# Optimization experiments

Measured on AMD Instinct MI355X. Metric: run time of the kernel, lower is better.

The kernel has to match this reference:

```python
import jax, jax.numpy as jnp
import numpy as np
from jax import lax

W_WIN = 7  # window size from init_kwargs


def _dwconv(x, k):
    """Depthwise 2D conv, SAME padding, kernel k: [C,1,kh,kw] (OIHW)."""
    C = x.shape[1]
    p = k.shape[-1] // 2
    return lax.conv_general_dilated(
        x, k, window_strides=(1, 1), padding=[(p, p), (p, p)],
        feature_group_count=C, dimension_numbers=("NCHW", "OIHW", "NCHW"))


def setup_inputs() -> dict:
    key = jax.random.key(0)
    ks = jax.random.split(key, 6)
    B, C, H, Wd = 1, 48, 56, 56
    x = jax.random.normal(ks[0], (B, C, H, Wd), dtype=jnp.float32)
    # small init scale keeps the softmax logits (dot/49) in a sane range
    w3 = jax.random.normal(ks[1], (C, 1, 3, 3), dtype=jnp.float32) * 0.1
    w5 = jax.random.normal(ks[2], (C, 1, 5, 5), dtype=jnp.float32) * 0.1
    w7 = jax.random.normal(ks[3], (C, 1, 7, 7), dtype=jnp.float32) * 0.1
    pw = jax.random.normal(ks[4], (C, 3 * C, 1, 1), dtype=jnp.float32) * 0.05
    pb = jax.random.normal(ks[5], (C,), dtype=jnp.float32) * 0.01
    return {"x": x, "w3": w3, "w5": w5, "w7": w7, "pw": pw, "pb": pb}


def reference(x, w3, w5, w7, pw, pb):
    B, C, H, Wd = x.shape
    w = W_WIN
    # multi-scale depthwise branch, concat on channels -> [B, 3C, H, W]
    y = jnp.concatenate([_dwconv(x, w3), _dwconv(x, w5), _dwconv(x, w7)], axis=1)
    pad_h = (-H) % w
    pad_w = (-Wd) % w
    if pad_h or pad_w:  # static Python ints -> jit-safe
        y = jnp.pad(y, ((0, 0), (0, 0), (0, pad_h), (0, pad_w)), mode="reflect")
    Hp, Wp = y.shape[2], y.shape[3]
    nH, nW = Hp // w, Wp // w
    C3 = 3 * C
    # equivalent to torch unfold(2,w,w).unfold(3,w,w).permute(0,1,2,4,3,5)
    # .reshape(B,3C,nH*nW,w*w): same row-major linearization
    yw = y.reshape(B, C3, nH * nW, w * w)
    # rows: (B, nH*nW, 3C) flattened -> N x (w*w)
    yf = yw.transpose(0, 2, 1, 3).reshape(B * nH * nW * C3, w * w)
    # full N x N self-attention over all rows (faithful to the original)
    attn = jax.nn.softmax((yf @ yf.T) / (w * w), axis=-1)
    y_hat = (attn @ yf).reshape(B, nH, nW, C3, w, w)
    y_hat = y_hat.transpose(0, 3, 1, 4, 2, 5).reshape(B, C3, nH * w, nW * w)
    y_hat = y_hat[:, :, :H, :Wd]
    # 1x1 projection 3C -> C, plus residual
    out = jnp.einsum("oi,bihw->bohw", pw[:, :, 0, 0], y_hat) + pb[None, :, None, None]
    return x + out
```

## Files before the change

kernel.cpp:

```cpp
#include <hip/hip_runtime.h>

typedef unsigned int uint;
typedef unsigned short ushort;
typedef __attribute__((ext_vector_type(8))) short bf16x8;
typedef __attribute__((ext_vector_type(4))) float f32x4;

#define C_IN   48
#define C3     144
#define HW     56
#define SSP    3136
#define DW     49
#define DPAD   64
#define NROWS  9216

#define NSPLIT 12
#define TPS    12

#define CSC 0.02944245f

#define YF_B    0
#define YFT_B   1179648
#define OPART_B 2359296
#define ESUM_B  (OPART_B + NSPLIT * DW * NROWS * 2)

__device__ __forceinline__ ushort f32_to_bf16_rne(float x) {
  uint b = __float_as_uint(x);
  b += 0x7fffu + ((b >> 16) & 1u);
  return (ushort)(b >> 16);
}
__device__ __forceinline__ float bf16_to_f32(ushort u) {
  return __uint_as_float(((uint)u) << 16);
}
__device__ __forceinline__ void async_copy16(const void* g, void* l) {
  __builtin_amdgcn_global_load_lds(
      (const __attribute__((address_space(1))) unsigned int*)g,
      (__attribute__((address_space(3))) unsigned int*)l, 16, 0, 0);
}

__global__ __launch_bounds__(256) void conv_kernel(
    const float* __restrict__ x, const float* __restrict__ w3,
    const float* __restrict__ w5, const float* __restrict__ w7,
    ushort* __restrict__ yf, ushort* __restrict__ yfT) {
  __shared__ ushort tile[4][64];
  const int tid = threadIdx.x;
  const int idx = blockIdx.x * 256 + tid;
  const int r = idx >> 6, t = idx & 63;
  const int rr = r & 3;
  const int r0 = r & ~3;

  ushort ov = 0;
  if (t < DW) {
    int g = r / C3, c3 = r - g * C3;
    int flat = g * DW + t;
    int h = flat / HW, w = flat - h * HW;
    int grp = c3 / C_IN, c = c3 - grp * C_IN;
    const float* wk; int ks;
    if (grp == 0)      { wk = w3 + c * 9;  ks = 3; }
    else if (grp == 1) { wk = w5 + c * 25; ks = 5; }
    else               { wk = w7 + c * 49; ks = 7; }
    int p = ks >> 1;
    const float* xc = x + c * SSP;
    float val = 0.f;
    for (int dy = 0; dy < ks; dy++) {
      int hy = h + dy - p;
      if (hy < 0 || hy >= HW) continue;
      const float* xr = xc + hy * HW;
      const float* wr = wk + dy * ks;
      for (int dx = 0; dx < ks; dx++) {
        int wx = w + dx - p;
        if (wx < 0 || wx >= HW) continue;
        val += xr[wx] * wr[dx];
      }
    }
    ov = f32_to_bf16_rne(val);
  }
  yf[idx] = ov;
  tile[rr][t] = ov;
  __syncthreads();

  if (tid < 64) {
    ushort4 v;
    if (tid == 56) {
      v.x = 0x3F80; v.y = 0x3F80; v.z = 0x3F80; v.w = 0x3F80;
    } else {
      v.x = tile[0][tid]; v.y = tile[1][tid];
      v.z = tile[2][tid]; v.w = tile[3][tid];
    }
    *(ushort4*)&yfT[tid * NROWS + r0] = v;
  }
}

__global__ __launch_bounds__(512, 4) void attn_kernel(
    const ushort* __restrict__ yf, const ushort* __restrict__ yfT,
    ushort* __restrict__ opart, float* __restrict__ esum_g) {
  __shared__ __align__(16) char smem[69632];

  const int tid = threadIdx.x;
  const int w = tid >> 6, lane = tid & 63;
  const int q = lane >> 4, c = lane & 15;
  const int m0 = blockIdx.x * 256 + w * 32;
  const int sp = blockIdx.y;
  ushort* Pm = (ushort*)(smem + 32768) + w * (32 * 72);

  bf16x8 qf[2][2];
#pragma unroll
  for (int mt = 0; mt < 2; mt++)
#pragma unroll
    for (int ds = 0; ds < 2; ds++) {
      bf16x8 raw = *(const bf16x8*)&yf[(m0 + mt * 16 + c) * 64 + ds * 32 + q * 8];
      short tmp[8];
#pragma unroll
      for (int j = 0; j < 8; j++)
        tmp[j] = (short)f32_to_bf16_rne(bf16_to_f32((ushort)raw[j]) * CSC);
      qf[mt][ds] = *(bf16x8*)tmp;
    }

  f32x4 o[4][2];
#pragma unroll
  for (int dt = 0; dt < 4; dt++)
#pragma unroll
    for (int mt = 0; mt < 2; mt++) o[dt][mt] = (f32x4)0.f;

  {
    const int k0 = (sp * TPS) * 64;
    async_copy16(yf + (k0 + lane) * 64 + w * 8, smem + w * 1024);
    async_copy16(yfT + lane * NROWS + k0 + w * 8, smem + 16384 + w * 1024);
  }
  __syncthreads();

  for (int it = 0; it < TPS; it++) {
    const int cur = it & 1;
    if (it + 1 < TPS) {
      const int k1 = (sp * TPS + it + 1) * 64;
      async_copy16(yf + (k1 + lane) * 64 + w * 8,
                   smem + (cur ^ 1) * 8192 + w * 1024);
      async_copy16(yfT + lane * NROWS + k1 + w * 8,
                   smem + 16384 + (cur ^ 1) * 8192 + w * 1024);
    }

    const char* Kb = smem + cur * 8192;
    const char* Vb = smem + 16384 + cur * 8192;

    f32x4 s[4][2];
#pragma unroll
    for (int nt = 0; nt < 4; nt++) {
      bf16x8 a0 = *(const bf16x8*)(Kb + q * 1024 + (nt * 16 + c) * 16);
      bf16x8 a1 = *(const bf16x8*)(Kb + (4 + q) * 1024 + (nt * 16 + c) * 16);
      s[nt][0] = (f32x4)0.f; s[nt][1] = (f32x4)0.f;
      s[nt][0] = __builtin_amdgcn_mfma_f32_16x16x32_bf16(a0, qf[0][0], s[nt][0], 0, 0, 0);
      s[nt][1] = __builtin_amdgcn_mfma_f32_16x16x32_bf16(a0, qf[1][0], s[nt][1], 0, 0, 0);
      s[nt][0] = __builtin_amdgcn_mfma_f32_16x16x32_bf16(a1, qf[0][1], s[nt][0], 0, 0, 0);
      s[nt][1] = __builtin_amdgcn_mfma_f32_16x16x32_bf16(a1, qf[1][1], s[nt][1], 0, 0, 0);
    }

#pragma unroll
    for (int nt = 0; nt < 4; nt++)
#pragma unroll
      for (int mt = 0; mt < 2; mt++) {
        f32x4 sv = s[nt][mt];
        float p0 = __builtin_amdgcn_exp2f(sv[0]);
        float p1 = __builtin_amdgcn_exp2f(sv[1]);
        float p2 = __builtin_amdgcn_exp2f(sv[2]);
        float p3 = __builtin_amdgcn_exp2f(sv[3]);
        uint d0 = (__float_as_uint(p0) >> 16) | (__float_as_uint(p1) & 0xffff0000u);
        uint d1 = (__float_as_uint(p2) >> 16) | (__float_as_uint(p3) & 0xffff0000u);
        *(uint2*)&Pm[(mt * 16 + c) * 72 + nt * 16 + q * 4] = make_uint2(d0, d1);
      }

    bf16x8 bp[2][2];
#pragma unroll
    for (int mt = 0; mt < 2; mt++)
#pragma unroll
      for (int nc = 0; nc < 2; nc++)
        bp[mt][nc] = *(const bf16x8*)&Pm[(mt * 16 + c) * 72 + nc * 32 + q * 8];
#pragma unroll
    for (int dt = 0; dt < 4; dt++) {
      bf16x8 v0 = *(const bf16x8*)(Vb + q * 1024 + (dt * 16 + c) * 16);
      bf16x8 v1 = *(const bf16x8*)(Vb + (4 + q) * 1024 + (dt * 16 + c) * 16);
      o[dt][0] = __builtin_amdgcn_mfma_f32_16x16x32_bf16(v0, bp[0][0], o[dt][0], 0, 0, 0);
      o[dt][1] = __builtin_amdgcn_mfma_f32_16x16x32_bf16(v0, bp[1][0], o[dt][1], 0, 0, 0);
      o[dt][0] = __builtin_amdgcn_mfma_f32_16x16x32_bf16(v1, bp[0][1], o[dt][0], 0, 0, 0);
      o[dt][1] = __builtin_amdgcn_mfma_f32_16x16x32_bf16(v1, bp[1][1], o[dt][1], 0, 0, 0);
    }

    if (it + 1 < TPS) __syncthreads();
  }

#pragma unroll
  for (int dt = 0; dt < 4; dt++)
#pragma unroll
    for (int mt = 0; mt < 2; mt++)
#pragma unroll
      for (int r = 0; r < 4; r++) {
        int d = dt * 16 + q * 4 + r;
        int m = m0 + mt * 16 + c;
        float v = o[dt][mt][r];
        if (d < DW) {
          opart[(sp * DW + d) * NROWS + m] = f32_to_bf16_rne(v);
        } else if (d == 56) {
          esum_g[sp * NROWS + m] = v;
        }
      }
}

__global__ __launch_bounds__(256) void fuse_pw_kernel(
    const ushort* __restrict__ opart, const float* __restrict__ esum_g,
    const float* __restrict__ x, const float* __restrict__ pw,
    const float* __restrict__ pb, float* __restrict__ out) {
  __shared__ float vb[7 * 145];
  __shared__ float inv_es[144];
  const int g = blockIdx.x, tch = blockIdx.y;
  const int t0 = tch * 7;
  const int tid = threadIdx.x;

  if (tid < 144) {
    int r = g * C3 + tid;
    float e = 0.f;
#pragma unroll
    for (int sp = 0; sp < NSPLIT; sp++) e += esum_g[sp * NROWS + r];
    inv_es[tid] = 1.f / e;
  }
  __syncthreads();

  for (int j = tid; j < 7 * 144; j += 256) {
    int tt = j / 144, i = j - tt * 144;
    int r = g * C3 + i, t = t0 + tt;
    float ov = 0.f;
#pragma unroll
    for (int sp = 0; sp < NSPLIT; sp++)
      ov += bf16_to_f32(opart[(sp * DW + t) * NROWS + r]);
    vb[tt * 145 + i] = ov * inv_es[i];
  }
  __syncthreads();

  for (int j = tid; j < C_IN * 7; j += 256) {
    int o = j / 7, tt = j - o * 7;
    int t = t0 + tt;
    const float* pwo = pw + o * C3;
    const float* vrow = &vb[tt * 145];
    float a0 = 0.f, a1 = 0.f, a2 = 0.f, a3 = 0.f;
#pragma unroll
    for (int i = 0; i < C3; i += 4) {
      float4 wv = *(const float4*)&pwo[i];
      a0 += wv.x * vrow[i];
      a1 += wv.y * vrow[i + 1];
      a2 += wv.z * vrow[i + 2];
      a3 += wv.w * vrow[i + 3];
    }
    float acc = (a0 + a1) + (a2 + a3);
    int nh = g >> 3, nw = g & 7;
    int th = t / 7, tw = t - th * 7;
    int oidx = o * SSP + (nh * 7 + th) * HW + (nw * 7 + tw);
    out[oidx] = x[oidx] + pb[o] + acc;
  }
}

extern "C" void kernel_launch(void* const* d_in, const int* in_sizes, int n_in,
                              void* d_out, int out_size, void* d_ws, size_t ws_size,
                              hipStream_t stream) {
  const float* x  = (const float*)d_in[0];
  const float* w3 = (const float*)d_in[1];
  const float* w5 = (const float*)d_in[2];
  const float* w7 = (const float*)d_in[3];
  const float* pw = (const float*)d_in[4];
  const float* pb = (const float*)d_in[5];
  float* out = (float*)d_out;
  char* ws = (char*)d_ws;

  ushort* yf    = (ushort*)(ws + YF_B);
  ushort* yfT   = (ushort*)(ws + YFT_B);
  ushort* opart = (ushort*)(ws + OPART_B);
  float*  esum  = (float*)(ws + ESUM_B);

  conv_kernel<<<(NROWS * DPAD) / 256, 256, 0, stream>>>(x, w3, w5, w7, yf, yfT);
  attn_kernel<<<dim3(NROWS / 256, NSPLIT), 512, 0, stream>>>(yf, yfT, opart, esum);
  fuse_pw_kernel<<<dim3(64, 7), 256, 0, stream>>>(opart, esum, x, pw, pb, out);
}
```

Before: 115.7 us.

## Keep softmax probabilities in registers by permuting V key columns

Removes the per-wave LDS round trip for the P matrix by packing exp2 results straight from MFMA accumulator layout into B-operand registers. To make that register layout match, the conv kernel writes yfT with a permuted key-column order inside each 64-key tile. LDS per block shrinks from 68 KB to 32 KB, which may allow more resident blocks, and the LDS write, read and wait traffic in the inner loop goes away. The cost is that the permutation must exactly match the MFMA lane mapping, and the two kernels now depend on each other's layout.

```diff
diff --git a/kernel.cpp b/kernel.cpp
--- a/kernel.cpp
+++ b/kernel.cpp
@@ -22,6 +22,7 @@
 #define YFT_B   1179648
 #define OPART_B 2359296
 #define ESUM_B  (OPART_B + NSPLIT * DW * NROWS * 2)
+
 
 __device__ __forceinline__ ushort f32_to_bf16_rne(float x) {
   uint b = __float_as_uint(x);
@@ -86,21 +87,22 @@
       v.x = tile[0][tid]; v.y = tile[1][tid];
       v.z = tile[2][tid]; v.w = tile[3][tid];
     }
-    *(ushort4*)&yfT[tid * NROWS + r0] = v;
+    const int k6 = r0 & 63;
+    const int pcol = (r0 & ~63) | (k6 & 35) | ((k6 & 12) << 1) | ((k6 & 16) >> 2);
+    *(ushort4*)&yfT[tid * NROWS + pcol] = v;
   }
 }
 
 __global__ __launch_bounds__(512, 4) void attn_kernel(
     const ushort* __restrict__ yf, const ushort* __restrict__ yfT,
     ushort* __restrict__ opart, float* __restrict__ esum_g) {
-  __shared__ __align__(16) char smem[69632];
+  __shared__ __align__(16) char smem[32768];
 
   const int tid = threadIdx.x;
   const int w = tid >> 6, lane = tid & 63;
   const int q = lane >> 4, c = lane & 15;
   const int m0 = blockIdx.x * 256 + w * 32;
   const int sp = blockIdx.y;
-  ushort* Pm = (ushort*)(smem + 32768) + w * (32 * 72);
 
   bf16x8 qf[2][2];
 #pragma unroll
@@ -141,38 +143,42 @@
     const char* Kb = smem + cur * 8192;
     const char* Vb = smem + 16384 + cur * 8192;
 
-    f32x4 s[4][2];
-#pragma unroll
-    for (int nt = 0; nt < 4; nt++) {
-      bf16x8 a0 = *(const bf16x8*)(Kb + q * 1024 + (nt * 16 + c) * 16);
-      bf16x8 a1 = *(const bf16x8*)(Kb + (4 + q) * 1024 + (nt * 16 + c) * 16);
-      s[nt][0] = (f32x4)0.f; s[nt][1] = (f32x4)0.f;
-      s[nt][0] = __builtin_amdgcn_mfma_f32_16x16x32_bf16(a0, qf[0][0], s[nt][0], 0, 0, 0);
-      s[nt][1] = __builtin_amdgcn_mfma_f32_16x16x32_bf16(a0, qf[1][0], s[nt][1], 0, 0, 0);
-      s[nt][0] = __builtin_amdgcn_mfma_f32_16x16x32_bf16(a1, qf[0][1], s[nt][0], 0, 0, 0);
-      s[nt][1] = __builtin_amdgcn_mfma_f32_16x16x32_bf16(a1, qf[1][1], s[nt][1], 0, 0, 0);
-    }
-
-#pragma unroll
-    for (int nt = 0; nt < 4; nt++)
+    bf16x8 bp[2][2];
+#pragma unroll
+    for (int nc = 0; nc < 2; nc++) {
+      f32x4 s[2][2];
+#pragma unroll
+      for (int h = 0; h < 2; h++) {
+        const int nt = nc * 2 + h;
+        bf16x8 a0 = *(const bf16x8*)(Kb + q * 1024 + (nt * 16 + c) * 16);
+        bf16x8 a1 = *(const bf16x8*)(Kb + (4 + q) * 1024 + (nt * 16 + c) * 16);
+#pragma unroll
+        for (int mt = 0; mt < 2; mt++) {
+          f32x4 acc = (f32x4)0.f;
+          acc = __builtin_amdgcn_mfma_f32_16x16x32_bf16(a0, qf[mt][0], acc, 0, 0, 0);
+          acc = __builtin_amdgcn_mfma_f32_16x16x32_bf16(a1, qf[mt][1], acc, 0, 0, 0);
+          s[h][mt] = acc;
+        }
+      }
 #pragma unroll
       for (int mt = 0; mt < 2; mt++) {
-        f32x4 sv = s[nt][mt];
-        float p0 = __builtin_amdgcn_exp2f(sv[0]);
-        float p1 = __builtin_amdgcn_exp2f(sv[1]);
-        float p2 = __builtin_amdgcn_exp2f(sv[2]);
-        float p3 = __builtin_amdgcn_exp2f(sv[3]);
-        uint d0 = (__float_as_uint(p0) >> 16) | (__float_as_uint(p1) & 0xffff0000u);
-        uint d1 = (__float_as_uint(p2) >> 16) | (__float_as_uint(p3) & 0xffff0000u);
-        *(uint2*)&Pm[(mt * 16 + c) * 72 + nt * 16 + q * 4] = make_uint2(d0, d1);
-      }
-
-    bf16x8 bp[2][2];
-#pragma unroll
-    for (int mt = 0; mt < 2; mt++)
-#pragma unroll
-      for (int nc = 0; nc < 2; nc++)
-        bp[mt][nc] = *(const bf16x8*)&Pm[(mt * 16 + c) * 72 + nc * 32 + q * 8];
+        uint u00 = __float_as_uint(__builtin_amdgcn_exp2f(s[0][mt][0]));
+        uint u01 = __float_as_uint(__builtin_amdgcn_exp2f(s[0][mt][1]));
+        uint u02 = __float_as_uint(__builtin_amdgcn_exp2f(s[0][mt][2]));
+        uint u03 = __float_as_uint(__builtin_amdgcn_exp2f(s[0][mt][3]));
+        uint u10 = __float_as_uint(__builtin_amdgcn_exp2f(s[1][mt][0]));
+        uint u11 = __float_as_uint(__builtin_amdgcn_exp2f(s[1][mt][1]));
+        uint u12 = __float_as_uint(__builtin_amdgcn_exp2f(s[1][mt][2]));
+        uint u13 = __float_as_uint(__builtin_amdgcn_exp2f(s[1][mt][3]));
+        uint4 t4;
+        t4.x = (u00 >> 16) | (u01 & 0xffff0000u);
+        t4.y = (u02 >> 16) | (u03 & 0xffff0000u);
+        t4.z = (u10 >> 16) | (u11 & 0xffff0000u);
+        t4.w = (u12 >> 16) | (u13 & 0xffff0000u);
+        bp[mt][nc] = *(bf16x8*)&t4;
+      }
+    }
+
 #pragma unroll
     for (int dt = 0; dt < 4; dt++) {
       bf16x8 v0 = *(const bf16x8*)(Vb + q * 1024 + (dt * 16 + c) * 16);
```

Measured after the change: 111.1 us. -3.9%, faster.
